# Performance work log

Hardware: AMD Instinct MI355X
Metric: run time of the kernel (lower is better)

Reference implementation:

```python
import jax, jax.numpy as jnp
import numpy as np
from jax import lax

EPS = 1e-5
COMMIT_W = 0.25

def conv2d(x, w, b):
    # x: [N,C,H,W], w: [O,I,3,3], SAME padding, stride 1
    y = lax.conv_general_dilated(x, w, (1, 1), 'SAME',
                                 dimension_numbers=('NCHW', 'OIHW', 'NCHW'))
    return y + b[None, :, None, None]

def batchnorm(x, gamma, beta):
    # training-mode batch norm over (N,H,W)
    m = jnp.mean(x, axis=(0, 2, 3), keepdims=True)
    v = jnp.var(x, axis=(0, 2, 3), keepdims=True)
    xhat = (x - m) * lax.rsqrt(v + EPS)
    return xhat * gamma[None, :, None, None] + beta[None, :, None, None]

def maxpool2(x):
    return lax.reduce_window(x, -jnp.inf, lax.max, (1, 1, 2, 2), (1, 1, 2, 2), 'VALID')

def setup_inputs() -> dict:
    key = jax.random.key(0)
    ks = jax.random.split(key, 8)
    B, C, H, W, D, K = 8, 3, 256, 256, 64, 1024
    return {
        'x': jax.random.normal(ks[0], (B, C, H, W), jnp.float32),
        'conv1_w': jax.random.normal(ks[1], (D, C, 3, 3), jnp.float32) * 0.05,
        'conv1_b': jnp.zeros((D,), jnp.float32),
        'bn1_gamma': jnp.ones((D,), jnp.float32),
        'bn1_beta': jnp.zeros((D,), jnp.float32),
        'embed': jax.random.normal(ks[2], (K, D), jnp.float32),
        'conv2_w': jax.random.normal(ks[3], (C, D, 3, 3), jnp.float32) * 0.05,
        'conv2_b': jnp.zeros((C,), jnp.float32),
        'bn2_gamma': jnp.ones((C,), jnp.float32),
        'bn2_beta': jnp.zeros((C,), jnp.float32),
    }

def reference(x, conv1_w, conv1_b, bn1_gamma, bn1_beta, embed,
              conv2_w, conv2_b, bn2_gamma, bn2_beta):
    # ---- encoder ----
    h = conv2d(x, conv1_w, conv1_b)
    h = batchnorm(h, bn1_gamma, bn1_beta)
    h = jax.nn.relu(h)
    h = maxpool2(h)                      # [B, D, H/2, W/2]
    B, D, Hh, Wh = h.shape
    # ---- vector quantize (accept_image_fmap) ----
    flat = jnp.transpose(h, (0, 2, 3, 1)).reshape(-1, D)   # [N, D]
    # squared euclidean distance to each code
    dist = (jnp.sum(flat * flat, axis=1, keepdims=True)
            - 2.0 * flat @ embed.T
            + jnp.sum(embed * embed, axis=1)[None, :])     # [N, K]
    idx = jnp.argmin(dist, axis=1)                          # [N]
    quant = embed[idx]                                      # gather [N, D]
    commit_loss = COMMIT_W * jnp.mean((lax.stop_gradient(quant) - flat) ** 2)
    # straight-through estimator
    quant_st = flat + lax.stop_gradient(quant - flat)
    q = jnp.transpose(quant_st.reshape(B, Hh, Wh, D), (0, 3, 1, 2))  # [B,D,Hh,Wh]
    indices = idx.reshape(B, Hh, Wh)
    # ---- decoder ----
    up = jnp.repeat(jnp.repeat(q, 2, axis=2), 2, axis=3)    # nearest x2
    y = conv2d(up, conv2_w, conv2_b)
    y = batchnorm(y, bn2_gamma, bn2_beta)
    y = jnp.tanh(y)
    return (y, indices, commit_loss)
```

## Files before the change

### kernel.cpp

```cpp
#include <hip/hip_runtime.h>
#include <hip/hip_bf16.h>
#include <math.h>

typedef unsigned int u32;
typedef unsigned short u16;
typedef __attribute__((ext_vector_type(8))) short short8v;
typedef __attribute__((ext_vector_type(4))) float f32x4;

#define HH 256
#define WW 256
#define HP 128
#define WP 128
#define NPTS (8*HP*WP)
#define NPIX 524288
#define Y_ELEMS (8*3*HH*WW)
#define IDX_OFF Y_ELEMS
#define LOSS_OFF (Y_ELEMS + NPTS)
#define MARGIN_MFMA 0.05f

__device__ __forceinline__ u32 bfr(float f) {
  u32 u = __float_as_uint(f);
  return (u + 0x7FFFu + ((u >> 16) & 1u)) >> 16;
}
__device__ __forceinline__ float bff(u32 h) { return __uint_as_float(h << 16); }

__global__ __launch_bounds__(256) void k1_fused(
    const float* __restrict__ x, const float* __restrict__ w1,
    const float* __restrict__ b1, double* __restrict__ part1,
    float* __restrict__ pooled) {
  __shared__ float wl[27*64];
  __shared__ float b1s[64];
  __shared__ float xs[3][4][68];
  __shared__ double sred[4][128];
  int t = threadIdx.x;
  for (int i = t; i < 27*64; i += 256) { int c = i & 63; int tap = i >> 6; wl[i] = w1[c*27 + tap]; }
  if (t < 64) b1s[t] = b1[t];
  int bx = blockIdx.x;
  int b = bx >> 9;
  int pid0 = (bx & 511) * 32;
  int py = pid0 >> 7;
  int px0 = pid0 & 127;
  int gcol0 = 2*px0 - 1, grow0 = 2*py - 1;
  for (int i = t; i < 816; i += 256) {
    int j = i % 68;
    int rr = (i / 68) & 3;
    int ic = i / 272;
    int col = gcol0 + j, row = grow0 + rr;
    float v = 0.f;
    if (col >= 0 && col < WW && row >= 0 && row < HH)
      v = x[((size_t)((b*3 + ic)*HH + row))*WW + col];
    xs[ic][rr][j] = v;
  }
  __syncthreads();
  int lpx = t >> 3;
  int co = (t & 7) * 8;
  float A0[8], A1[8], C0[8], C1[8];
  #pragma unroll
  for (int c = 0; c < 8; ++c) { float bb = b1s[co + c]; A0[c] = bb; A1[c] = bb; C0[c] = bb; C1[c] = bb; }
  #pragma unroll
  for (int ic = 0; ic < 3; ++ic) {
    #pragma unroll
    for (int dy = 0; dy < 3; ++dy) {
      const float* wb = wl + (size_t)((ic*3 + dy)*3)*64 + co;
      int j0 = 2*lpx;
      float xa0 = xs[ic][dy][j0+0], xa1 = xs[ic][dy][j0+1], xa2 = xs[ic][dy][j0+2], xa3 = xs[ic][dy][j0+3];
      float xc0 = xs[ic][dy+1][j0+0], xc1 = xs[ic][dy+1][j0+1], xc2 = xs[ic][dy+1][j0+2], xc3 = xs[ic][dy+1][j0+3];
      #pragma unroll
      for (int c = 0; c < 8; ++c) {
        float w0 = wb[c], w1v = wb[64 + c], w2v = wb[128 + c];
        A0[c] = fmaf(xa0, w0, fmaf(xa1, w1v, fmaf(xa2, w2v, A0[c])));
        A1[c] = fmaf(xa1, w0, fmaf(xa2, w1v, fmaf(xa3, w2v, A1[c])));
        C0[c] = fmaf(xc0, w0, fmaf(xc1, w1v, fmaf(xc2, w2v, C0[c])));
        C1[c] = fmaf(xc1, w0, fmaf(xc2, w1v, fmaf(xc3, w2v, C1[c])));
      }
    }
  }
  double s[8], q[8];
  float m[8];
  #pragma unroll
  for (int c = 0; c < 8; ++c) {
    double dA0 = (double)A0[c], dA1 = (double)A1[c], dC0 = (double)C0[c], dC1 = (double)C1[c];
    double s_ = 0.0;
    s_ += dA0 + dA1;
    double q_ = fma(dA0, dA0, 0.0);
    q_ = fma(dA1, dA1, q_);
    float m_ = fmaxf(-3.4e38f, fmaxf(A0[c], A1[c]));
    s_ += dC0 + dC1;
    q_ = fma(dC0, dC0, q_);
    q_ = fma(dC1, dC1, q_);
    m_ = fmaxf(m_, fmaxf(C0[c], C1[c]));
    s[c] = s_; q[c] = q_; m[c] = m_;
  }
  int pid = pid0 + lpx;
  size_t p = (size_t)b*16384 + pid;
  *(float4*)(pooled + p*64 + co)     = make_float4(m[0], m[1], m[2], m[3]);
  *(float4*)(pooled + p*64 + co + 4) = make_float4(m[4], m[5], m[6], m[7]);
  #pragma unroll 1
  for (int c = 0; c < 8; ++c) {
    #pragma unroll
    for (int st = 8; st < 64; st <<= 1) {
      s[c] += __shfl_xor(s[c], st, 64);
      q[c] += __shfl_xor(q[c], st, 64);
    }
  }
  int w = t >> 6;
  if ((t & 63) < 8) {
    #pragma unroll
    for (int c = 0; c < 8; ++c) {
      sred[w][co + c] = s[c];
      sred[w][64 + co + c] = q[c];
    }
  }
  __syncthreads();
  if (t < 128)
    part1[(size_t)bx*128 + t] = (sred[0][t] + sred[1][t]) + (sred[2][t] + sred[3][t]);
}

__global__ __launch_bounds__(256) void k2_reduce_bn1(
    const double* __restrict__ part1, const float* __restrict__ gamma,
    const float* __restrict__ beta, double* __restrict__ sAB1) {
  int c = blockIdx.x, t = threadIdx.x;
  double s = 0.0, q = 0.0;
  for (int i = t; i < 4096; i += 256) {
    const double* p = part1 + (size_t)i*128;
    s += p[c];
    q += p[64 + c];
  }
  __shared__ double ls[256], lq[256];
  ls[t] = s; lq[t] = q;
  __syncthreads();
  for (int o = 128; o > 0; o >>= 1) {
    if (t < o) { ls[t] += ls[t+o]; lq[t] += lq[t+o]; }
    __syncthreads();
  }
  if (t == 0) {
    double mean = ls[0] / (double)NPIX;
    double var  = lq[0] / (double)NPIX - mean*mean;
    double A = (double)gamma[c] / sqrt(var + 1e-5);
    sAB1[c] = A;
    sAB1[64 + c] = (double)beta[c] - mean*A;
  }
}

__global__ void kE_prep(const float* __restrict__ embed, char* __restrict__ epack,
                        double* __restrict__ enormd, float* __restrict__ enf,
                        u32* __restrict__ flagcnt,
                        const float* __restrict__ w2, float* __restrict__ weff) {
  int bxx = blockIdx.x;
  if (bxx >= 4) {
    int e = (bxx - 4)*256 + threadIdx.x;
    if (e >= 16*64*4) return;
    int oc = e & 3;
    int ic = (e >> 2) & 63;
    int combo = e >> 8;
    if (oc == 3) { weff[e] = 0.f; return; }
    int bq = combo & 1, a = (combo >> 1) & 1, ex = (combo >> 2) & 1, ey = combo >> 3;
    int rs = (a == 0) ? 0 : (ey == 0 ? 1 : 2);
    int rc = ((a ^ ey) != 0) ? 2 : 1;
    int cs = (bq == 0) ? 0 : (ex == 0 ? 1 : 2);
    int cc = ((bq ^ ex) != 0) ? 2 : 1;
    float ssum = 0.f;
    for (int i = 0; i < rc; ++i)
      for (int j = 0; j < cc; ++j)
        ssum += w2[((oc*64 + ic)*3 + (rs + i))*3 + (cs + j)];
    weff[e] = ssum;
    return;
  }
  if (bxx == 0 && threadIdx.x == 0) flagcnt[0] = 0u;
  int k = bxx*256 + threadIdx.x;
  const float4* e4 = (const float4*)(embed + (size_t)k*64);
  u32 hw[32], lw[32];
  double s0 = 0.0, s1 = 0.0;
  #pragma unroll
  for (int i = 0; i < 16; ++i) {
    float4 v = e4[i];
    float f0 = v.x, f1 = v.y, f2 = v.z, f3 = v.w;
    s0 = fma((double)f0, (double)f0, s0); s1 = fma((double)f1, (double)f1, s1);
    s0 = fma((double)f2, (double)f2, s0); s1 = fma((double)f3, (double)f3, s1);
    u32 h0 = bfr(f0), h1 = bfr(f1), h2 = bfr(f2), h3 = bfr(f3);
    u32 l0 = bfr(f0 - bff(h0)), l1 = bfr(f1 - bff(h1));
    u32 l2 = bfr(f2 - bff(h2)), l3 = bfr(f3 - bff(h3));
    hw[2*i]   = h0 | (h1 << 16);
    hw[2*i+1] = h2 | (h3 << 16);
    lw[2*i]   = l0 | (l1 << 16);
    lw[2*i+1] = l2 | (l3 << 16);
  }
  char* tb = epack + (size_t)(k >> 4)*4096 + (size_t)(k & 15)*16;
  #pragma unroll
  for (int g = 0; g < 4; ++g) {
    *(uint4*)(tb + 0*1024 + g*256) = make_uint4(hw[4*g+0], hw[4*g+1], hw[4*g+2], hw[4*g+3]);
    *(uint4*)(tb + 1*1024 + g*256) = make_uint4(hw[16+4*g+0], hw[16+4*g+1], hw[16+4*g+2], hw[16+4*g+3]);
    *(uint4*)(tb + 2*1024 + g*256) = make_uint4(lw[4*g+0], lw[4*g+1], lw[4*g+2], lw[4*g+3]);
    *(uint4*)(tb + 3*1024 + g*256) = make_uint4(lw[16+4*g+0], lw[16+4*g+1], lw[16+4*g+2], lw[16+4*g+3]);
  }
  double e = s0 + s1;
  enormd[k] = e;
  enf[k] = (float)e;
}

__global__ __launch_bounds__(256) void kp_proj(
    const float* __restrict__ embed, const float* __restrict__ weff,
    float* __restrict__ proj) {
  int e = blockIdx.x*256 + threadIdx.x;
  int k = e >> 6;
  int slot = e & 63;
  int combo = slot >> 2, oc = slot & 3;
  if (oc == 3) { proj[e] = 0.f; return; }
  const float* er = embed + (size_t)k*64;
  const float* wc = weff + combo*256 + oc;
  float s0 = 0.f, s1 = 0.f;
  #pragma unroll 8
  for (int ic = 0; ic < 64; ic += 2) {
    s0 = fmaf(er[ic],     wc[ic*4],     s0);
    s1 = fmaf(er[ic + 1], wc[ic*4 + 4], s1);
  }
  proj[e] = s0 + s1;
}

#define MFMA_BF16 __builtin_amdgcn_mfma_f32_16x16x32_bf16
#define PROC_T(ntv) { \
  int code = (ntv)*16 + col; \
  float en2 = senf[code];    \
  f32x4 accA0={en2,en2,en2,en2}, accA1={0.f,0.f,0.f,0.f}; \
  f32x4 accB0={en2,en2,en2,en2}, accB1={0.f,0.f,0.f,0.f}; \
  accA0 = MFMA_BF16(aA_h0, b_h0, accA0, 0, 0, 0); \
  accA1 = MFMA_BF16(aA_h1, b_h1, accA1, 0, 0, 0); \
  accB0 = MFMA_BF16(aB_h0, b_h0, accB0, 0, 0, 0); \
  accB1 = MFMA_BF16(aB_h1, b_h1, accB1, 0, 0, 0); \
  accA0 = MFMA_BF16(aA_l0, b_h0, accA0, 0, 0, 0); \
  accA1 = MFMA_BF16(aA_l1, b_h1, accA1, 0, 0, 0); \
  accB0 = MFMA_BF16(aB_l0, b_h0, accB0, 0, 0, 0); \
  accB1 = MFMA_BF16(aB_l1, b_h1, accB1, 0, 0, 0); \
  accA0 = MFMA_BF16(aA_h0, b_l0, accA0, 0, 0, 0); \
  accA1 = MFMA_BF16(aA_h1, b_l1, accA1, 0, 0, 0); \
  accB0 = MFMA_BF16(aB_h0, b_l0, accB0, 0, 0, 0); \
  accB1 = MFMA_BF16(aB_h1, b_l1, accB1, 0, 0, 0); \
  _Pragma("unroll") \
  for (int j = 0; j < 4; ++j) { \
    float mA = accA0[j] + accA1[j]; \
    bool cA = mA > bestA[j]; \
    b2A[j] = fmaxf(b2A[j], fminf(mA, bestA[j])); \
    bestA[j] = fmaxf(bestA[j], mA); \
    idxA[j] = cA ? code : idxA[j]; \
    float mB = accB0[j] + accB1[j]; \
    bool cB = mB > bestB[j]; \
    b2B[j] = fmaxf(b2B[j], fminf(mB, bestB[j])); \
    bestB[j] = fmaxf(bestB[j], mB); \
    idxB[j] = cB ? code : idxB[j]; \
  } \
}
#define PROC_LDS(bb, ntv) { \
  short8v b_h0 = *(const short8v*)((bb) + 0*1024 + lane*16); \
  short8v b_h1 = *(const short8v*)((bb) + 1*1024 + lane*16); \
  short8v b_l0 = *(const short8v*)((bb) + 2*1024 + lane*16); \
  short8v b_l1 = *(const short8v*)((bb) + 3*1024 + lane*16); \
  PROC_T(ntv); \
}

__global__ __launch_bounds__(256) void kB_mfma(
    const float* __restrict__ pooled, const double* __restrict__ sAB1,
    const char* __restrict__ epack, const float* __restrict__ enf,
    int* __restrict__ idxbuf, float* __restrict__ out_f, double* __restrict__ lossq,
    u32* __restrict__ flagcnt, u32* __restrict__ flagids) {
  __shared__ float senf[1024];
  __shared__ char shbuf[32768];
  __shared__ float fnp[256];
  __shared__ float fnsum[128];
  __shared__ float sAs[64], sBs[64];
  __shared__ double wred[4];
  int t = threadIdx.x;
  for (int i = t; i < 1024; i += 256) senf[i] = -0.5f * enf[i];
  if (t < 64) { sAs[t] = (float)sAB1[t]; sBs[t] = (float)sAB1[64 + t]; }
  __syncthreads();
  {
    int lp = t >> 1, h = t & 1, cb = h*32;
    int p = blockIdx.x*128 + lp;
    const float4* src = (const float4*)(pooled + (size_t)p*64 + cb);
    float fn = 0.f;
    u32 hw[16], lw[16];
    #pragma unroll
    for (int i = 0; i < 8; ++i) {
      float4 v = src[i];
      float f0 = fmaxf(fmaf(v.x, sAs[cb+4*i+0], sBs[cb+4*i+0]), 0.f);
      float f1 = fmaxf(fmaf(v.y, sAs[cb+4*i+1], sBs[cb+4*i+1]), 0.f);
      float f2 = fmaxf(fmaf(v.z, sAs[cb+4*i+2], sBs[cb+4*i+2]), 0.f);
      float f3 = fmaxf(fmaf(v.w, sAs[cb+4*i+3], sBs[cb+4*i+3]), 0.f);
      fn = fmaf(f0, f0, fn); fn = fmaf(f1, f1, fn);
      fn = fmaf(f2, f2, fn); fn = fmaf(f3, f3, fn);
      u32 h0 = bfr(f0), h1 = bfr(f1), h2 = bfr(f2), h3 = bfr(f3);
      u32 l0 = bfr(f0 - bff(h0)), l1 = bfr(f1 - bff(h1));
      u32 l2 = bfr(f2 - bff(h2)), l3 = bfr(f3 - bff(h3));
      hw[2*i]   = h0 | (h1 << 16);
      hw[2*i+1] = h2 | (h3 << 16);
      lw[2*i]   = l0 | (l1 << 16);
      lw[2*i+1] = l2 | (l3 << 16);
    }
    uint4* dh = (uint4*)(shbuf + (size_t)lp*256 + h*64);
    uint4* dl = (uint4*)(shbuf + (size_t)lp*256 + 128 + h*64);
    #pragma unroll
    for (int i = 0; i < 4; ++i) dh[i] = make_uint4(hw[4*i], hw[4*i+1], hw[4*i+2], hw[4*i+3]);
    #pragma unroll
    for (int i = 0; i < 4; ++i) dl[i] = make_uint4(lw[4*i], lw[4*i+1], lw[4*i+2], lw[4*i+3]);
    fnp[t] = fn;
  }
  __syncthreads();
  if ((t & 1) == 0) fnsum[t >> 1] = fnp[t] + fnp[t + 1];
  int lane = t & 63;
  int col = lane & 15, g = lane >> 4;
  int w = t >> 6;
  const char* fbA = shbuf + (size_t)(w*32 + col)*256 + 16*g;
  const char* fbB = shbuf + (size_t)(w*32 + 16 + col)*256 + 16*g;
  short8v aA_h0 = *(const short8v*)(fbA);
  short8v aA_h1 = *(const short8v*)(fbA + 64);
  short8v aA_l0 = *(const short8v*)(fbA + 128);
  short8v aA_l1 = *(const short8v*)(fbA + 192);
  short8v aB_h0 = *(const short8v*)(fbB);
  short8v aB_h1 = *(const short8v*)(fbB + 64);
  short8v aB_l0 = *(const short8v*)(fbB + 128);
  short8v aB_l1 = *(const short8v*)(fbB + 192);
  __syncthreads();
  char (*btile)[4][4096] = (char (*)[4][4096])shbuf;
  float bestA[4], b2A[4], bestB[4], b2B[4];
  int idxA[4], idxB[4];
  #pragma unroll
  for (int j = 0; j < 4; ++j) {
    bestA[j] = -3.4e38f; b2A[j] = -3.4e38f; idxA[j] = 0;
    bestB[j] = -3.4e38f; b2B[j] = -3.4e38f; idxB[j] = 0;
  }
  #pragma unroll
  for (int k = 0; k < 4; ++k)
    *(uint4*)(&btile[0][k][t*16]) = *(const uint4*)(epack + (size_t)k*4096 + (size_t)t*16);
  __syncthreads();
  #pragma unroll 1
  for (int ng = 0; ng < 16; ++ng) {
    int cur = ng & 1;
    uint4 stg0, stg1, stg2, stg3;
    if (ng < 15) {
      const char* base = epack + (size_t)(4*ng + 4)*4096 + (size_t)t*16;
      stg0 = *(const uint4*)(base);
      stg1 = *(const uint4*)(base + 4096);
      stg2 = *(const uint4*)(base + 8192);
      stg3 = *(const uint4*)(base + 12288);
    }
    PROC_LDS(&btile[cur][0][0], 4*ng + 0);
    PROC_LDS(&btile[cur][1][0], 4*ng + 1);
    PROC_LDS(&btile[cur][2][0], 4*ng + 2);
    PROC_LDS(&btile[cur][3][0], 4*ng + 3);
    if (ng < 15) {
      *(uint4*)(&btile[cur ^ 1][0][t*16]) = stg0;
      *(uint4*)(&btile[cur ^ 1][1][t*16]) = stg1;
      *(uint4*)(&btile[cur ^ 1][2][t*16]) = stg2;
      *(uint4*)(&btile[cur ^ 1][3][t*16]) = stg3;
    }
    __syncthreads();
  }
  double lsum = 0.0;
  #pragma unroll
  for (int grp = 0; grp < 2; ++grp) {
    #pragma unroll
    for (int j = 0; j < 4; ++j) {
      float b  = (grp == 0) ? bestA[j] : bestB[j];
      float s2 = (grp == 0) ? b2A[j]   : b2B[j];
      int  id  = (grp == 0) ? idxA[j]  : idxB[j];
      #pragma unroll
      for (int m = 1; m < 16; m <<= 1) {
        float ob  = __shfl_xor(b, m, 64);
        float os2 = __shfl_xor(s2, m, 64);
        int  oid  = __shfl_xor(id, m, 64);
        s2 = fmaxf(fmaxf(s2, os2), fminf(b, ob));
        if (ob > b || (ob == b && oid < id)) { b = ob; id = oid; }
      }
      if (col == 0) {
        int lpt = w*32 + grp*16 + g*4 + j;
        int p = blockIdx.x*128 + lpt;
        idxbuf[p] = id;
        out_f[IDX_OFF + p] = (float)id;
        lsum += (double)fmaf(-2.f, b, fnsum[lpt]);
        if (b - s2 <= 0.5f*MARGIN_MFMA) { u32 pos = atomicAdd(flagcnt, 1u); flagids[pos] = (u32)p; }
      }
    }
  }
  #pragma unroll
  for (int m = 1; m < 64; m <<= 1) lsum += __shfl_xor(lsum, m, 64);
  if (lane == 0) wred[w] = lsum;
  __syncthreads();
  if (t == 0) lossq[blockIdx.x] = (wred[0] + wred[1]) + (wred[2] + wred[3]);
}

__global__ __launch_bounds__(64) void kC_fallback(
    const float* __restrict__ x, const float* __restrict__ w1,
    const float* __restrict__ b1, const double* __restrict__ sAB1,
    const float* __restrict__ embed, const double* __restrict__ enormd,
    const u32* __restrict__ flagcnt, const u32* __restrict__ flagids,
    int* __restrict__ idxbuf, float* __restrict__ out_f) {
  __shared__ double fd[64];
  int lane = threadIdx.x;
  double wv[27];
  #pragma unroll
  for (int i = 0; i < 27; ++i) wv[i] = (double)w1[lane*27 + i];
  double bias = (double)b1[lane];
  double A = sAB1[lane], B = sAB1[64 + lane];
  u32 n = flagcnt[0];
  for (u32 i = blockIdx.x; i < n; i += gridDim.x) {
    int p = (int)flagids[i];
    int b = p >> 14, py = (p >> 7) & 127, px = p & 127;
    double mx = -1e300;
    #pragma unroll
    for (int ry = 0; ry < 2; ++ry) {
      #pragma unroll
      for (int cx = 0; cx < 2; ++cx) {
        double a = bias;
        int yy = 2*py + ry, xx = 2*px + cx;
        #pragma unroll
        for (int ic = 0; ic < 3; ++ic) {
          #pragma unroll
          for (int dy = 0; dy < 3; ++dy) {
            int ryy = yy + dy - 1;
            if (ryy >= 0 && ryy < HH) {
              const float* row = x + ((size_t)((b*3 + ic)*HH + ryy))*WW;
              #pragma unroll
              for (int dxx = 0; dxx < 3; ++dxx) {
                int xc = xx + dxx - 1;
                if (xc >= 0 && xc < WW) a = fma((double)row[xc], wv[(ic*3 + dy)*3 + dxx], a);
              }
            }
          }
        }
        mx = fmax(mx, a);
      }
    }
    fd[lane] = fmax(fma(mx, A, B), 0.0);
    __syncthreads();
    double bd = 1e300; int bk = 1 << 20;
    for (int kk = 0; kk < 16; ++kk) {
      int k = kk*64 + lane;
      const float* e = embed + (size_t)k*64;
      double e0=0,e1=0,e2=0,e3=0;
      #pragma unroll
      for (int d = 0; d < 16; ++d) {
        e0 = fma(fd[4*d+0], (double)e[4*d+0], e0);
        e1 = fma(fd[4*d+1], (double)e[4*d+1], e1);
        e2 = fma(fd[4*d+2], (double)e[4*d+2], e2);
        e3 = fma(fd[4*d+3], (double)e[4*d+3], e3);
      }
      double dist = fma(-2.0, (e0+e1)+(e2+e3), enormd[k]);
      if (dist < bd) { bd = dist; bk = k; }
    }
    #pragma unroll
    for (int st = 1; st < 64; st <<= 1) {
      double od = __shfl_xor(bd, st, 64);
      int ok = __shfl_xor(bk, st, 64);
      if (od < bd || (od == bd && ok < bk)) { bd = od; bk = ok; }
    }
    if (lane == 0) {
      idxbuf[p] = bk;
      out_f[IDX_OFF + p] = (float)bk;
    }
    __syncthreads();
  }
}

__global__ __launch_bounds__(256) void k5b_loss(const double* __restrict__ lossq, float* __restrict__ out) {
  __shared__ double red[256];
  int t = threadIdx.x;
  red[t] = (lossq[t] + lossq[t + 256]) + (lossq[t + 512] + lossq[t + 768]);
  __syncthreads();
  for (int o = 128; o > 0; o >>= 1) { if (t < o) red[t] += red[t+o]; __syncthreads(); }
  if (t == 0) {
    double loss = 0.25 * red[0] / (double)((size_t)NPTS * 64);
    out[LOSS_OFF] = (float)loss;
  }
}

template<int MODE>
__global__ __launch_bounds__(256) void conv2_body(
    const int* __restrict__ idxbuf, const float* __restrict__ proj,
    const float* __restrict__ c2b, const float* __restrict__ sAB2,
    float* __restrict__ part2, float* __restrict__ ybuf, float* __restrict__ yout) {
  __shared__ float xw[4][6];
  int t = threadIdx.x;
  int bx = blockIdx.x;
  int b = bx >> 6;
  int tile = bx & 63;
  int px = (tile & 1)*64 + (t & 63);
  int py = (tile >> 1)*4 + (t >> 6);
  const int* idxb = idxbuf + b*HP*WP;
  float acc[12];
  #pragma unroll
  for (int i = 0; i < 12; ++i) acc[i] = 0.f;
  #pragma unroll
  for (int r = 0; r < 3; ++r) {
    int cy = py - 1 + r;
    bool vy = (cy >= 0) && (cy < HP);
    #pragma unroll
    for (int s = 0; s < 3; ++s) {
      int cx = px - 1 + s;
      if (!(vy && (cx >= 0) && (cx < WP))) continue;
      int ii = idxb[cy*WP + cx];
      const float4* pr = (const float4*)(proj + (size_t)ii*64);
      #pragma unroll
      for (int rp = 0; rp < ((r==1) ? 2 : 1); ++rp) {
        const int pa = (r==0) ? 0 : (r==2) ? 1 : rp;
        const int ca = (r==0) ? 0 : (r==2) ? 1 : (1-rp);
        #pragma unroll
        for (int sp = 0; sp < ((s==1) ? 2 : 1); ++sp) {
          const int pb = (s==0) ? 0 : (s==2) ? 1 : sp;
          const int cb = (s==0) ? 0 : (s==2) ? 1 : (1-sp);
          float4 v = pr[pa*8 + pb*4 + ca*2 + cb];
          int ob = (pa*2 + pb)*3;
          acc[ob+0] += v.x;
          acc[ob+1] += v.y;
          acc[ob+2] += v.z;
        }
      }
    }
  }
  if (MODE == 2) {
    #pragma unroll
    for (int pa = 0; pa < 2; ++pa) {
      int yy = 2*py + pa;
      #pragma unroll
      for (int pb = 0; pb < 2; ++pb) {
        int xx = 2*px + pb;
        int ob = (pa*2 + pb)*3;
        float v0 = tanhf(fmaf(acc[ob+0], sAB2[0], sAB2[4]));
        float v1 = tanhf(fmaf(acc[ob+1], sAB2[1], sAB2[5]));
        float v2 = tanhf(fmaf(acc[ob+2], sAB2[2], sAB2[6]));
        yout[((size_t)(b*3 + 0)*HH + yy)*WW + xx] = v0;
        yout[((size_t)(b*3 + 1)*HH + yy)*WW + xx] = v1;
        yout[((size_t)(b*3 + 2)*HH + yy)*WW + xx] = v2;
      }
    }
  } else {
    float s0=0.f,s1=0.f,s2=0.f, q0=0.f,q1=0.f,q2=0.f;
    #pragma unroll
    for (int pa = 0; pa < 2; ++pa) {
      int yy = 2*py + pa;
      #pragma unroll
      for (int pb = 0; pb < 2; ++pb) {
        int xx = 2*px + pb;
        int ob = (pa*2 + pb)*3;
        float v0 = acc[ob+0] + c2b[0], v1 = acc[ob+1] + c2b[1], v2 = acc[ob+2] + c2b[2];
        s0 += v0; s1 += v1; s2 += v2;
        q0 = fmaf(v0, v0, q0); q1 = fmaf(v1, v1, q1); q2 = fmaf(v2, v2, q2);
        if (MODE == 1) {
          ybuf[((size_t)(b*3 + 0)*HH + yy)*WW + xx] = v0;
          ybuf[((size_t)(b*3 + 1)*HH + yy)*WW + xx] = v1;
          ybuf[((size_t)(b*3 + 2)*HH + yy)*WW + xx] = v2;
        }
      }
    }
    float sv[3] = {s0, s1, s2}, qv2[3] = {q0, q1, q2};
    #pragma unroll
    for (int oc = 0; oc < 3; ++oc) {
      float v = sv[oc], q = qv2[oc];
      #pragma unroll
      for (int m = 1; m < 64; m <<= 1) { v += __shfl_xor(v, m, 64); q += __shfl_xor(q, m, 64); }
      if ((t & 63) == 0) { xw[t >> 6][oc] = v; xw[t >> 6][3 + oc] = q; }
    }
    __syncthreads();
    if (t == 0) {
      #pragma unroll
      for (int i = 0; i < 6; ++i)
        part2[bx*6 + i] = (xw[0][i] + xw[1][i]) + (xw[2][i] + xw[3][i]);
    }
  }
}

__global__ __launch_bounds__(256) void k7_reduce_bn2(
    const float* __restrict__ part2, const float* __restrict__ g2,
    const float* __restrict__ bt2, const float* __restrict__ c2b,
    float* __restrict__ sAB2, int fold_bias) {
  int t = threadIdx.x;
  int w = t >> 6, lane = t & 63;
  if (w >= 3) return;
  double s = 0.0, q = 0.0;
  for (int i = lane; i < 512; i += 64) {
    s += (double)part2[i*6 + w];
    q += (double)part2[i*6 + 3 + w];
  }
  #pragma unroll
  for (int m = 1; m < 64; m <<= 1) { s += __shfl_xor(s, m, 64); q += __shfl_xor(q, m, 64); }
  if (lane == 0) {
    double mean = s / (double)NPIX;
    double var  = q / (double)NPIX - mean*mean;
    double A = (double)g2[w] / sqrt(var + 1e-5);
    double Bc = (double)bt2[w] - mean*A;
    if (fold_bias) Bc += (double)c2b[w]*A;
    sAB2[w] = (float)A;
    sAB2[4 + w] = (float)Bc;
  }
}

__global__ __launch_bounds__(256) void k8_apply(
    const float* __restrict__ ybuf, const float* __restrict__ sAB2,
    float* __restrict__ yout) {
  int i4 = blockIdx.x*256 + threadIdx.x;
  int i = i4 * 4;
  int oc = (i >> 16) % 3;
  float A = sAB2[oc], B = sAB2[4 + oc];
  float4 v = *(const float4*)(ybuf + i);
  float4 r;
  r.x = tanhf(fmaf(v.x, A, B));
  r.y = tanhf(fmaf(v.y, A, B));
  r.z = tanhf(fmaf(v.z, A, B));
  r.w = tanhf(fmaf(v.w, A, B));
  *(float4*)(yout + i) = r;
}

extern "C" void kernel_launch(void* const* d_in, const int* in_sizes, int n_in,
                              void* d_out, int out_size, void* d_ws, size_t ws_size,
                              hipStream_t stream) {
  const float* x   = (const float*)d_in[0];
  const float* w1  = (const float*)d_in[1];
  const float* b1  = (const float*)d_in[2];
  const float* g1  = (const float*)d_in[3];
  const float* bt1 = (const float*)d_in[4];
  const float* emb = (const float*)d_in[5];
  const float* w2  = (const float*)d_in[6];
  const float* b2  = (const float*)d_in[7];
  const float* g2  = (const float*)d_in[8];
  const float* bt2 = (const float*)d_in[9];
  float* out = (float*)d_out;

  char* ws = (char*)d_ws;
  float*  pooled  = (float*) (ws);
  double* part1   = (double*)(ws + 33554432);
  char*   epack   =          (ws + 33554432);
  float*  proj    = (float*) (ws + 33816576);
  int*    idxbuf  = (int*)   (ws + 37748736);
  u32*    flagids = (u32*)   (ws + 38273024);
  u32*    flagcnt = (u32*)   (ws + 38797312);
  float*  part2   = (float*) (ws + 38799424);
  double* sAB1    = (double*)(ws + 38811712);
  float*  sAB2    = (float*) (ws + 38812736);
  double* enormd  = (double*)(ws + 38812800);
  float*  enf     = (float*) (ws + 38820992);
  float*  weff    = (float*) (ws + 38825088);
  double* lossq   = (double*)(ws + 38841472);
  float*  ybuf    = (float*) (ws + 38849664);
  bool use_ybuf = (ws_size >= (size_t)45141120);

  hipLaunchKernelGGL(k1_fused, dim3(4096), dim3(256), 0, stream, x, w1, b1, part1, pooled);
  hipLaunchKernelGGL(k2_reduce_bn1, dim3(64), dim3(256), 0, stream, part1, g1, bt1, sAB1);
  hipLaunchKernelGGL(kE_prep, dim3(20), dim3(256), 0, stream, emb, epack, enormd, enf, flagcnt, w2, weff);
  hipLaunchKernelGGL(kp_proj, dim3(256), dim3(256), 0, stream, emb, weff, proj);
  hipLaunchKernelGGL(kB_mfma, dim3(1024), dim3(256), 0, stream, pooled, sAB1, (const char*)epack,
                     enf, idxbuf, out, lossq, flagcnt, flagids);
  hipLaunchKernelGGL(kC_fallback, dim3(2048), dim3(64), 0, stream, x, w1, b1, sAB1, emb, enormd,
                     flagcnt, flagids, idxbuf, out);
  hipLaunchKernelGGL(k5b_loss, dim3(1), dim3(256), 0, stream, lossq, out);
  if (use_ybuf) {
    hipLaunchKernelGGL((conv2_body<1>), dim3(512), dim3(256), 0, stream, idxbuf, proj, b2, sAB2, part2, ybuf, out);
    hipLaunchKernelGGL(k7_reduce_bn2, dim3(1), dim3(256), 0, stream, part2, g2, bt2, b2, sAB2, 0);
    hipLaunchKernelGGL(k8_apply, dim3(1536), dim3(256), 0, stream, ybuf, sAB2, out);
  } else {
    hipLaunchKernelGGL((conv2_body<0>), dim3(512), dim3(256), 0, stream, idxbuf, proj, b2, sAB2, part2, ybuf, out);
    hipLaunchKernelGGL(k7_reduce_bn2, dim3(1), dim3(256), 0, stream, part2, g2, bt2, b2, sAB2, 1);
    hipLaunchKernelGGL((conv2_body<2>), dim3(512), dim3(256), 0, stream, idxbuf, proj, b2, sAB2, part2, ybuf, out);
  }
}
```

Baseline: 206.5 us.

## Fold loss reduction into fallback kernel, add MFMA priority and med3 tracking

The standalone loss-reduction kernel is removed. Its work now runs in an extra last block of the fallback kernel, and the fallback loop stride is adjusted to match. Separately, the MFMA section of the nearest-code search is wrapped in s_setprio to raise wave priority during matrix ops. The second-best tracking uses a single fmed3 instead of a fmin/fmax pair. Together these aim to save one kernel launch and a few VALU instructions in the hot loop, at the cost of a serial 64-lane reduction in one block.

```diff
diff --git a/kernel.cpp b/kernel.cpp
--- a/kernel.cpp
+++ b/kernel.cpp
@@ -223,6 +223,7 @@
   float en2 = senf[code];    \
   f32x4 accA0={en2,en2,en2,en2}, accA1={0.f,0.f,0.f,0.f}; \
   f32x4 accB0={en2,en2,en2,en2}, accB1={0.f,0.f,0.f,0.f}; \
+  __builtin_amdgcn_s_setprio(1); \
   accA0 = MFMA_BF16(aA_h0, b_h0, accA0, 0, 0, 0); \
   accA1 = MFMA_BF16(aA_h1, b_h1, accA1, 0, 0, 0); \
   accB0 = MFMA_BF16(aB_h0, b_h0, accB0, 0, 0, 0); \
@@ -235,16 +236,17 @@
   accA1 = MFMA_BF16(aA_h1, b_l1, accA1, 0, 0, 0); \
   accB0 = MFMA_BF16(aB_h0, b_l0, accB0, 0, 0, 0); \
   accB1 = MFMA_BF16(aB_h1, b_l1, accB1, 0, 0, 0); \
+  __builtin_amdgcn_s_setprio(0); \
   _Pragma("unroll") \
   for (int j = 0; j < 4; ++j) { \
     float mA = accA0[j] + accA1[j]; \
     bool cA = mA > bestA[j]; \
-    b2A[j] = fmaxf(b2A[j], fminf(mA, bestA[j])); \
+    b2A[j] = __builtin_amdgcn_fmed3f(b2A[j], mA, bestA[j]);   \
     bestA[j] = fmaxf(bestA[j], mA); \
     idxA[j] = cA ? code : idxA[j]; \
     float mB = accB0[j] + accB1[j]; \
     bool cB = mB > bestB[j]; \
-    b2B[j] = fmaxf(b2B[j], fminf(mB, bestB[j])); \
+    b2B[j] = __builtin_amdgcn_fmed3f(b2B[j], mB, bestB[j]); \
     bestB[j] = fmaxf(bestB[j], mB); \
     idxB[j] = cB ? code : idxB[j]; \
   } \
@@ -392,16 +394,26 @@
     const float* __restrict__ b1, const double* __restrict__ sAB1,
     const float* __restrict__ embed, const double* __restrict__ enormd,
     const u32* __restrict__ flagcnt, const u32* __restrict__ flagids,
-    int* __restrict__ idxbuf, float* __restrict__ out_f) {
+    int* __restrict__ idxbuf, float* __restrict__ out_f,
+    const double* __restrict__ lossq) {
+  int lane = threadIdx.x;
+  if (blockIdx.x == gridDim.x - 1) {
+    double s = 0.0;
+    for (int i = lane; i < 1024; i += 64) s += lossq[i];
+    #pragma unroll
+    for (int st = 1; st < 64; st <<= 1) s += __shfl_xor(s, st, 64);
+    if (lane == 0) out_f[LOSS_OFF] = (float)(0.25 * s / (double)((size_t)NPTS * 64));
+    return;
+  }
   __shared__ double fd[64];
-  int lane = threadIdx.x;
   double wv[27];
   #pragma unroll
   for (int i = 0; i < 27; ++i) wv[i] = (double)w1[lane*27 + i];
   double bias = (double)b1[lane];
   double A = sAB1[lane], B = sAB1[64 + lane];
   u32 n = flagcnt[0];
-  for (u32 i = blockIdx.x; i < n; i += gridDim.x) {
+  u32 stride = gridDim.x - 1;
+  for (u32 i = blockIdx.x; i < n; i += stride) {
     int p = (int)flagids[i];
     int b = p >> 14, py = (p >> 7) & 127, px = p & 127;
     double mx = -1e300;
@@ -460,18 +472,6 @@
   }
 }
 
-__global__ __launch_bounds__(256) void k5b_loss(const double* __restrict__ lossq, float* __restrict__ out) {
-  __shared__ double red[256];
-  int t = threadIdx.x;
-  red[t] = (lossq[t] + lossq[t + 256]) + (lossq[t + 512] + lossq[t + 768]);
-  __syncthreads();
-  for (int o = 128; o > 0; o >>= 1) { if (t < o) red[t] += red[t+o]; __syncthreads(); }
-  if (t == 0) {
-    double loss = 0.25 * red[0] / (double)((size_t)NPTS * 64);
-    out[LOSS_OFF] = (float)loss;
-  }
-}
-
 template<int MODE>
 __global__ __launch_bounds__(256) void conv2_body(
     const int* __restrict__ idxbuf, const float* __restrict__ proj,
@@ -647,9 +647,8 @@
   hipLaunchKernelGGL(kp_proj, dim3(256), dim3(256), 0, stream, emb, weff, proj);
   hipLaunchKernelGGL(kB_mfma, dim3(1024), dim3(256), 0, stream, pooled, sAB1, (const char*)epack,
                      enf, idxbuf, out, lossq, flagcnt, flagids);
-  hipLaunchKernelGGL(kC_fallback, dim3(2048), dim3(64), 0, stream, x, w1, b1, sAB1, emb, enormd,
-                     flagcnt, flagids, idxbuf, out);
-  hipLaunchKernelGGL(k5b_loss, dim3(1), dim3(256), 0, stream, lossq, out);
+  hipLaunchKernelGGL(kC_fallback, dim3(2049), dim3(64), 0, stream, x, w1, b1, sAB1, emb, enormd,
+                     flagcnt, flagids, idxbuf, out, lossq);
   if (use_ybuf) {
     hipLaunchKernelGGL((conv2_body<1>), dim3(512), dim3(256), 0, stream, idxbuf, proj, b2, sAB2, part2, ybuf, out);
     hipLaunchKernelGGL(k7_reduce_bn2, dim3(1), dim3(256), 0, stream, part2, g2, bt2, b2, sAB2, 0);
```

Result: no change. 202.8 us (-1.8%).
